# Optimization experiments

Hardware: AMD Instinct MI355X
Metric: run time of the kernel (lower is better)

The kernel has to match this reference:

```python
import jax, jax.numpy as jnp
import numpy as np

N = 50000      # nodes
E = 800000     # edges (avg degree 16)
F_IN = 128     # in_channels
H = 4          # heads
C = 32         # hidden_channels (per-head out)
L = 3          # num_layers
HC = H * C     # 128 == F_IN so residuals are active


def _layer_norm(x, g, b):
    mu = jnp.mean(x, axis=-1, keepdims=True)
    var = jnp.mean(jnp.square(x - mu), axis=-1, keepdims=True)
    return (x - mu) * jax.lax.rsqrt(var + 1e-5) * g + b


def _gatv2(x, W_l, b_l, W_r, b_r, att, src, dst, concat):
    # GATv2Conv (PyG semantics, eval mode: no dropout)
    xl = (x @ W_l + b_l).reshape(-1, H, C)   # source-side transform  [N,H,C]
    xr = (x @ W_r + b_r).reshape(-1, H, C)   # target-side transform  [N,H,C]
    e = jax.nn.leaky_relu(xl[src] + xr[dst], 0.2)          # [E,H,C]
    alpha = jnp.einsum('ehc,hc->eh', e, att)               # [E,H]
    # segment softmax over incoming edges of each dst node
    m = jax.ops.segment_max(alpha, dst, num_segments=N)    # [N,H]
    a = jnp.exp(alpha - m[dst])
    den = jax.ops.segment_sum(a, dst, num_segments=N) + 1e-16
    a = a / den[dst]
    out = jax.ops.segment_sum(xl[src] * a[:, :, None], dst, num_segments=N)  # [N,H,C]
    if concat:
        return out.reshape(N, HC)
    return out.mean(axis=1)


def setup_inputs() -> dict:
    key = jax.random.key(0)
    ks = jax.random.split(key, 6)
    s = 0.05
    return {
        "x": jax.random.normal(ks[0], (N, F_IN), jnp.float32),
        "edge_index": jax.random.randint(ks[1], (2, E), 0, N, dtype=jnp.int32),
        # all 3 layers have in=128, out=H*C=128 for the linears
        "Wl": jax.random.normal(ks[2], (L, F_IN, HC), jnp.float32) * s,
        "bl": jnp.zeros((L, HC), jnp.float32),
        "Wr": jax.random.normal(ks[3], (L, F_IN, HC), jnp.float32) * s,
        "br": jnp.zeros((L, HC), jnp.float32),
        "att": jax.random.normal(ks[4], (L, H, C), jnp.float32) * s,
        "out_bias01": jnp.zeros((2, HC), jnp.float32),   # concat layers 0,1
        "out_bias2": jnp.zeros((C,), jnp.float32),       # mean layer 2
        "ln_g01": jnp.ones((2, HC), jnp.float32),
        "ln_b01": jnp.zeros((2, HC), jnp.float32),
        "ln_g2": jnp.ones((C,), jnp.float32),
        "ln_b2": jnp.zeros((C,), jnp.float32),
    }


def reference(x, edge_index, Wl, bl, Wr, br, att,
              out_bias01, out_bias2, ln_g01, ln_b01, ln_g2, ln_b2):
    src, dst = edge_index[0], edge_index[1]
    for i in range(L):
        x_in = x
        concat = i < L - 1
        h = _gatv2(x, Wl[i], bl[i], Wr[i], br[i], att[i], src, dst, concat)
        if concat:
            h = h + out_bias01[i]
            h = _layer_norm(h, ln_g01[i], ln_b01[i])
        else:
            h = h + out_bias2
            h = _layer_norm(h, ln_g2, ln_b2)
        h = jax.nn.relu(h)  # dropout omitted (eval mode)
        if i > 0 and h.shape == x_in.shape:
            h = h + x_in
        x = h
    return x
```

## Files before the change

kernel.cpp:

```cpp
#include <hip/hip_runtime.h>
#include <math.h>


#define DPP_QP_XOR1 0xB1
#define DPP_QP_XOR2 0x4E
#define DPP_ROW_MIRROR 0x140
#define DPP_ROW_HALF_MIRROR 0x141

template <int CTRL>
__device__ __forceinline__ float dpp_add(float v) {
    int x = __builtin_amdgcn_update_dpp(0, __float_as_int(v), CTRL, 0xf, 0xf, true);
    return v + __int_as_float(x);
}

__device__ __forceinline__ unsigned bf16s(float f) {
    unsigned u = __float_as_uint(f);
    return (u + 0x7fffu + ((u >> 16) & 1u)) >> 16;
}

typedef __bf16 bf16x8 __attribute__((ext_vector_type(8)));
typedef float f32x4 __attribute__((ext_vector_type(4)));
typedef float f32x2 __attribute__((ext_vector_type(2)));


__global__ void hist_kernel(const int* __restrict__ dst, int* __restrict__ deg, int E) {
    int e = blockIdx.x * blockDim.x + threadIdx.x;
    if (e < E) atomicAdd(&deg[dst[e]], 1);
}

__global__ __launch_bounds__(256) void block_reduce_kernel(
    const int* __restrict__ deg, int* __restrict__ bsum, int Nn) {
    const int t = threadIdx.x;
    const int idx = blockIdx.x * 256 + t;
    int v = (idx < Nn) ? deg[idx] : 0;
#pragma unroll
    for (int k = 1; k <= 32; k <<= 1) v += __shfl_xor(v, k);
    __shared__ int ws[4];
    if ((t & 63) == 0) ws[t >> 6] = v;
    __syncthreads();
    if (t == 0) bsum[blockIdx.x] = ws[0] + ws[1] + ws[2] + ws[3];
}

__global__ __launch_bounds__(256) void scan_partials_kernel(
    const int* __restrict__ bsum, int* __restrict__ boff, int nb) {
    const int t = threadIdx.x;
    int v = (t < nb) ? bsum[t] : 0;
    __shared__ int s[256];
    s[t] = v;
    __syncthreads();
    for (int off = 1; off < 256; off <<= 1) {
        int u = (t >= off) ? s[t - off] : 0;
        __syncthreads();
        s[t] += u;
        __syncthreads();
    }
    if (t < nb) boff[t] = s[t] - v;
}

__global__ __launch_bounds__(256) void block_scan_write_kernel(
    const int* __restrict__ deg, const int* __restrict__ boff,
    int* __restrict__ row_start, int Nn) {
    const int t = threadIdx.x;
    const int idx = blockIdx.x * 256 + t;
    int v = (idx < Nn) ? deg[idx] : 0;
    __shared__ int s[256];
    s[t] = v;
    __syncthreads();
    for (int off = 1; off < 256; off <<= 1) {
        int u = (t >= off) ? s[t - off] : 0;
        __syncthreads();
        s[t] += u;
        __syncthreads();
    }
    if (idx < Nn) row_start[idx] = s[t] - v + boff[blockIdx.x];
}

__global__ void init_bucket_cursor(const int* __restrict__ row_start,
                                   int* __restrict__ bucket_cursor, int NB) {
    int b = blockIdx.x * blockDim.x + threadIdx.x;
    if (b < NB) bucket_cursor[b] = row_start[b * 128];
}

#define EPB 8192
#define MAXB 512

__global__ __launch_bounds__(256) void bin_kernel(
    const int* __restrict__ src, const int* __restrict__ dst,
    int* __restrict__ bucket_cursor, unsigned* __restrict__ ebuf,
    int E, int NB)
{
    __shared__ int hist[MAXB], lbase[MAXB], gbase[MAXB], cur[MAXB];
    __shared__ int sscan[256];
    __shared__ unsigned stage[EPB];
    const int t = threadIdx.x;
    const int base = blockIdx.x * EPB;
    const int cnt = min(EPB, E - base);

    for (int b = t; b < MAXB; b += 256) hist[b] = 0;
    __syncthreads();
    for (int idx = t; idx < cnt; idx += 256)
        atomicAdd(&hist[dst[base + idx] >> 7], 1);
    __syncthreads();
    {
        const int a = hist[2 * t], b = hist[2 * t + 1];
        sscan[t] = a + b;
        __syncthreads();
        for (int off = 1; off < 256; off <<= 1) {
            int u = (t >= off) ? sscan[t - off] : 0;
            __syncthreads();
            sscan[t] += u;
            __syncthreads();
        }
        const int ex = sscan[t] - (a + b);
        lbase[2 * t] = ex;
        lbase[2 * t + 1] = ex + a;
    }
    __syncthreads();
    for (int b = t; b < NB; b += 256) {
        const int c = hist[b];
        gbase[b] = (c > 0) ? atomicAdd(&bucket_cursor[b], c) : 0;
        cur[b] = lbase[b];
    }
    __syncthreads();
    for (int idx = t; idx < cnt; idx += 256) {
        const int d = dst[base + idx];
        const int bk = d >> 7;
        const int lp = atomicAdd(&cur[bk], 1);
        stage[lp] = (unsigned)src[base + idx] | ((unsigned)(d & 127) << 16)
                  | ((unsigned)bk << 23);
    }
    __syncthreads();
    for (int idx = t; idx < cnt; idx += 256) {
        const unsigned v = stage[idx];
        const int bk = v >> 23;
        ebuf[gbase[bk] + (idx - lbase[bk])] = v;
    }
}

#define BCAP 3072

__global__ __launch_bounds__(256) void place_kernel(
    const unsigned* __restrict__ ebuf, const int* __restrict__ row_start,
    int* __restrict__ src_sorted, int E, int Nn, int NB)
{
    __shared__ int cur[128];
    __shared__ unsigned short stage[BCAP];
    const int b = blockIdx.x;
    const int t = threadIdx.x;
    const int node0 = b * 128;
    const int start = row_start[node0];
    const int end = (b == NB - 1) ? E : row_start[node0 + 128];
    const int cnt = end - start;

    if (t < 128) {
        const int n = node0 + t;
        cur[t] = (n < Nn) ? row_start[n] - start : 0;
    }
    __syncthreads();

    if (cnt <= BCAP) {
        for (int i = t; i < cnt; i += 256) {
            const unsigned v = ebuf[start + i];
            const int lp = atomicAdd(&cur[(v >> 16) & 127], 1);
            stage[lp] = (unsigned short)(v & 0xffffu);
        }
        __syncthreads();
        for (int i = t; i < cnt; i += 256)
            src_sorted[start + i] = (int)stage[i];
    } else {
        for (int i = t; i < cnt; i += 256) {
            const unsigned v = ebuf[start + i];
            const int lp = atomicAdd(&cur[(v >> 16) & 127], 1);
            src_sorted[start + lp] = (int)(v & 0xffffu);
        }
    }
}


__global__ void build_bt_kernel(const float* __restrict__ Wl, const float* __restrict__ Wr,
                                unsigned short* __restrict__ Bt, int total) {
    int idx = blockIdx.x * blockDim.x + threadIdx.x;
    if (idx >= total) return;
    const int k = idx & 127;
    const int n = (idx >> 7) & 255;
    const int l = idx >> 15;
    const float v = (n < 128) ? Wl[l * 16384 + k * 128 + n]
                              : Wr[l * 16384 + k * 128 + (n - 128)];
    Bt[idx] = (unsigned short)bf16s(v);
}

__global__ void cvt_kernel(const float* __restrict__ x, unsigned* __restrict__ xb, int n8) {
    int idx = blockIdx.x * blockDim.x + threadIdx.x;
    if (idx >= n8) return;
    const float4 a = reinterpret_cast<const float4*>(x)[idx * 2];
    const float4 b = reinterpret_cast<const float4*>(x)[idx * 2 + 1];
    uint4 o;
    o.x = bf16s(a.x) | (bf16s(a.y) << 16);
    o.y = bf16s(a.z) | (bf16s(a.w) << 16);
    o.z = bf16s(b.x) | (bf16s(b.y) << 16);
    o.w = bf16s(b.z) | (bf16s(b.w) << 16);
    reinterpret_cast<uint4*>(xb)[idx] = o;
}


__global__ __launch_bounds__(256) void gemm_mfma(
    const unsigned short* __restrict__ Xb, const unsigned short* __restrict__ Bt,
    const float* __restrict__ bl, const float* __restrict__ br,
    unsigned short* __restrict__ XLb, unsigned short* __restrict__ XRb, int Nn)
{
    const int t = threadIdx.x;
    const int lane = t & 63;
    const int w = t >> 6;
    const int n0 = w * 64;
    const int l15 = lane & 15;
    const int kg = lane >> 4;
    const int rowBase = blockIdx.x * 32;

    f32x4 acc[2][4] = {};

    int ra[2];
    ra[0] = min(rowBase + l15, Nn - 1);
    ra[1] = min(rowBase + 16 + l15, Nn - 1);

#pragma unroll
    for (int ks = 0; ks < 4; ++ks) {
        const int k0 = ks * 32 + kg * 8;
        bf16x8 a[2];
        a[0] = *reinterpret_cast<const bf16x8*>(Xb + (size_t)ra[0] * 128 + k0);
        a[1] = *reinterpret_cast<const bf16x8*>(Xb + (size_t)ra[1] * 128 + k0);
#pragma unroll
        for (int nt = 0; nt < 4; ++nt) {
            const int col = n0 + nt * 16 + l15;
            const bf16x8 b = *reinterpret_cast<const bf16x8*>(Bt + (size_t)col * 128 + k0);
            acc[0][nt] = __builtin_amdgcn_mfma_f32_16x16x32_bf16(a[0], b, acc[0][nt], 0, 0, 0);
            acc[1][nt] = __builtin_amdgcn_mfma_f32_16x16x32_bf16(a[1], b, acc[1][nt], 0, 0, 0);
        }
    }

    const bool isXL = (w < 2);
#pragma unroll
    for (int mt = 0; mt < 2; ++mt) {
#pragma unroll
        for (int nt = 0; nt < 4; ++nt) {
            const int col = n0 + nt * 16 + l15;
            const float bv = isXL ? bl[col] : br[col - 128];
#pragma unroll
            for (int r = 0; r < 4; ++r) {
                const int row = rowBase + mt * 16 + kg * 4 + r;
                if (row >= Nn) continue;
                const float v = acc[mt][nt][r] + bv;
                if (isXL) XLb[(size_t)row * 128 + col] = (unsigned short)bf16s(v);
                else      XRb[(size_t)row * 128 + (col - 128)] = (unsigned short)bf16s(v);
            }
        }
    }
}


__device__ __forceinline__ void unpack8(const uint4 q, f32x2* v) {
    v[0] = f32x2{__uint_as_float(q.x << 16), __uint_as_float(q.x & 0xffff0000u)};
    v[1] = f32x2{__uint_as_float(q.y << 16), __uint_as_float(q.y & 0xffff0000u)};
    v[2] = f32x2{__uint_as_float(q.z << 16), __uint_as_float(q.z & 0xffff0000u)};
    v[3] = f32x2{__uint_as_float(q.w << 16), __uint_as_float(q.w & 0xffff0000u)};
}

__device__ __forceinline__ void edge_accum(const uint4 q, const f32x2* xr, const f32x2* av,
                                           const bool dead, float& wsum, f32x2* acc) {
    f32x2 xl[4];
    unpack8(q, xl);
    f32x2 pd = {0.f, 0.f};
#pragma unroll
    for (int j = 0; j < 4; ++j) {
        f32x2 tt = xl[j] + xr[j];
        const f32x2 u = tt * 0.2f;
        tt.x = fmaxf(tt.x, u.x);
        tt.y = fmaxf(tt.y, u.y);
        pd += tt * av[j];
    }
    float part = pd.x + pd.y;
    part = dpp_add<DPP_QP_XOR1>(part);
    part = dpp_add<DPP_QP_XOR2>(part);
    if (dead) part = -INFINITY;
    const float e = __expf(part);
    wsum += e;
    const f32x2 e2 = {e, e};
#pragma unroll
    for (int j = 0; j < 4; ++j) acc[j] += e2 * xl[j];
}

template <int MODE>
__global__ __launch_bounds__(256) void aggregate_kernel(
    const unsigned* __restrict__ XLb, const unsigned* __restrict__ XRb,
    const int* __restrict__ row_start, const int* __restrict__ deg,
    const int* __restrict__ src_sorted,
    const float* __restrict__ att, const float* __restrict__ obias,
    const float* __restrict__ lng, const float* __restrict__ lnb,
    const float* __restrict__ resid, float* __restrict__ out,
    unsigned* __restrict__ outb, int Nn)
{
    const int lane = threadIdx.x & 63;
    const int wid = threadIdx.x >> 6;
    const int node = blockIdx.x * 4 + wid;
    if (node >= Nn) return;
    const int g = lane >> 4;
    const int i = lane & 15;
    const int c0 = i * 8;

    f32x2 xr[4], av[4];
    {
        const uint4 qr = reinterpret_cast<const uint4*>(XRb)[(size_t)node * 16 + i];
        unpack8(qr, xr);
        const float4 c = *reinterpret_cast<const float4*>(att + c0);
        const float4 d = *reinterpret_cast<const float4*>(att + c0 + 4);
        av[0] = f32x2{c.x, c.y}; av[1] = f32x2{c.z, c.w};
        av[2] = f32x2{d.x, d.y}; av[3] = f32x2{d.z, d.w};
    }

    f32x2 acc[4] = {};
    float wsum = 0.f;

    const int p0 = row_start[node];
    const int dg = deg[node];
    const int p1 = p0 + dg;

    if (dg > 0) {
        int sA = src_sorted[min(p0 + g, p1 - 1)];
        int sB = src_sorted[min(p0 + 4 + g, p1 - 1)];
        for (int p = p0; p < p1; p += 8) {
            const int sAn = src_sorted[min(p + 8 + g, p1 - 1)];
            const int sBn = src_sorted[min(p + 12 + g, p1 - 1)];
            const uint4 qA = reinterpret_cast<const uint4*>(XLb)[(size_t)sA * 16 + i];
            const uint4 qB = reinterpret_cast<const uint4*>(XLb)[(size_t)sB * 16 + i];
            edge_accum(qA, xr, av, p + g >= p1, wsum, acc);
            if (p + 4 < p1)
                edge_accum(qB, xr, av, p + 4 + g >= p1, wsum, acc);
            sA = sAn;
            sB = sBn;
        }
    }

    wsum += __shfl_xor(wsum, 16); wsum += __shfl_xor(wsum, 32);
    float o[8];
#pragma unroll
    for (int j = 0; j < 4; ++j) { o[2 * j] = acc[j].x; o[2 * j + 1] = acc[j].y; }
#pragma unroll
    for (int j = 0; j < 8; ++j) {
        o[j] += __shfl_xor(o[j], 16);
        o[j] += __shfl_xor(o[j], 32);
    }

    const float inv = 1.f / (wsum + 1e-16f);
#pragma unroll
    for (int j = 0; j < 8; ++j) o[j] *= inv;

    if (MODE < 2) {
        float v[8], d[8];
        float s = 0.f;
#pragma unroll
        for (int j = 0; j < 8; ++j) { v[j] = o[j] + obias[c0 + j]; s += v[j]; }
        s = dpp_add<DPP_QP_XOR1>(s); s = dpp_add<DPP_QP_XOR2>(s);
        s = dpp_add<DPP_ROW_MIRROR>(s); s = dpp_add<DPP_ROW_HALF_MIRROR>(s);
        const float mu = s * (1.f / 128.f);
        float q = 0.f;
#pragma unroll
        for (int j = 0; j < 8; ++j) { d[j] = v[j] - mu; q = fmaf(d[j], d[j], q); }
        q = dpp_add<DPP_QP_XOR1>(q); q = dpp_add<DPP_QP_XOR2>(q);
        q = dpp_add<DPP_ROW_MIRROR>(q); q = dpp_add<DPP_ROW_HALF_MIRROR>(q);
        const float rstd = rsqrtf(q * (1.f / 128.f) + 1e-5f);
        float h[8];
#pragma unroll
        for (int j = 0; j < 8; ++j)
            h[j] = fmaxf(d[j] * rstd * lng[c0 + j] + lnb[c0 + j], 0.f);
        if (MODE == 1) {
            const float4 r0 = *reinterpret_cast<const float4*>(resid + (size_t)node * 128 + c0);
            const float4 r1 = *reinterpret_cast<const float4*>(resid + (size_t)node * 128 + c0 + 4);
            h[0] += r0.x; h[1] += r0.y; h[2] += r0.z; h[3] += r0.w;
            h[4] += r1.x; h[5] += r1.y; h[6] += r1.z; h[7] += r1.w;
        }
        if (g == 0) {
            if (MODE == 0) {
                *reinterpret_cast<float4*>(out + (size_t)node * 128 + c0) =
                    make_float4(h[0], h[1], h[2], h[3]);
                *reinterpret_cast<float4*>(out + (size_t)node * 128 + c0 + 4) =
                    make_float4(h[4], h[5], h[6], h[7]);
            }
            uint4 pb;
            pb.x = bf16s(h[0]) | (bf16s(h[1]) << 16);
            pb.y = bf16s(h[2]) | (bf16s(h[3]) << 16);
            pb.z = bf16s(h[4]) | (bf16s(h[5]) << 16);
            pb.w = bf16s(h[6]) | (bf16s(h[7]) << 16);
            reinterpret_cast<uint4*>(outb)[(size_t)node * 16 + i] = pb;
        }
    } else {
#pragma unroll
        for (int j = 0; j < 8; ++j) {
            o[j] += __shfl_xor(o[j], 4);
            o[j] += __shfl_xor(o[j], 8);
            o[j] *= 0.25f;
        }
        const int cb = (i & 3) * 8;
        float v[8], d[8];
        float s = 0.f;
#pragma unroll
        for (int j = 0; j < 8; ++j) { v[j] = o[j] + obias[cb + j]; s += v[j]; }
        s = dpp_add<DPP_QP_XOR1>(s); s = dpp_add<DPP_QP_XOR2>(s);
        const float mu = s * (1.f / 32.f);
        float q = 0.f;
#pragma unroll
        for (int j = 0; j < 8; ++j) { d[j] = v[j] - mu; q = fmaf(d[j], d[j], q); }
        q = dpp_add<DPP_QP_XOR1>(q); q = dpp_add<DPP_QP_XOR2>(q);
        const float rstd = rsqrtf(q * (1.f / 32.f) + 1e-5f);
        float h[8];
#pragma unroll
        for (int j = 0; j < 8; ++j)
            h[j] = fmaxf(d[j] * rstd * lng[cb + j] + lnb[cb + j], 0.f);
        if (lane < 4) {
            *reinterpret_cast<float4*>(out + (size_t)node * 32 + cb) =
                make_float4(h[0], h[1], h[2], h[3]);
            *reinterpret_cast<float4*>(out + (size_t)node * 32 + cb + 4) =
                make_float4(h[4], h[5], h[6], h[7]);
        }
    }
}

extern "C" void kernel_launch(void* const* d_in, const int* in_sizes, int n_in,
                              void* d_out, int out_size, void* d_ws, size_t ws_size,
                              hipStream_t stream)
{
    const float* x    = (const float*)d_in[0];
    const int*   ei   = (const int*)d_in[1];
    const float* Wl   = (const float*)d_in[2];
    const float* bl   = (const float*)d_in[3];
    const float* Wr   = (const float*)d_in[4];
    const float* br   = (const float*)d_in[5];
    const float* att  = (const float*)d_in[6];
    const float* ob01 = (const float*)d_in[7];
    const float* ob2  = (const float*)d_in[8];
    const float* lg01 = (const float*)d_in[9];
    const float* lb01 = (const float*)d_in[10];
    const float* lg2  = (const float*)d_in[11];
    const float* lb2  = (const float*)d_in[12];
    float* outp = (float*)d_out;

    const int Nn = in_sizes[0] / 128;
    const int E  = in_sizes[1] / 2;
    const int* srcI = ei;
    const int* dstI = ei + E;
    const int NB = (Nn + 127) / 128;

    char* ws = (char*)d_ws;
    size_t off = 0;
    auto alloc = [&](size_t bytes) {
        void* p = ws + off;
        off += (bytes + 255) & ~(size_t)255;
        return p;
    };
    unsigned short* Xb0  = (unsigned short*)alloc((size_t)Nn * 128 * 2);
    unsigned short* XLb  = (unsigned short*)alloc((size_t)Nn * 128 * 2);
    unsigned short* XRb  = (unsigned short*)alloc((size_t)Nn * 128 * 2);
    float* bufA          = (float*)alloc((size_t)Nn * 128 * 4);
    unsigned short* bufAb = (unsigned short*)alloc((size_t)Nn * 128 * 2);
    unsigned short* bufBb = (unsigned short*)alloc((size_t)Nn * 128 * 2);
    unsigned short* Bt   = (unsigned short*)alloc((size_t)3 * 256 * 128 * 2);
    int*   deg           = (int*)alloc((size_t)Nn * 4);
    int*   row_start     = (int*)alloc((size_t)Nn * 4);
    int*   src_sorted    = (int*)alloc((size_t)E * 4);
    unsigned* ebuf       = (unsigned*)alloc((size_t)E * 4);
    int*   bucket_cur    = (int*)alloc((size_t)MAXB * 4);
    int*   bsum          = (int*)alloc(1024 * 4);
    int*   boff          = (int*)alloc(1024 * 4);
    (void)ws_size;

    const int nb = (Nn + 255) / 256;

    hipMemsetAsync(deg, 0, (size_t)Nn * 4, stream);
    cvt_kernel<<<(Nn * 16 + 255) / 256, 256, 0, stream>>>(x, (unsigned*)Xb0, Nn * 16);
    hist_kernel<<<(E + 255) / 256, 256, 0, stream>>>(dstI, deg, E);
    build_bt_kernel<<<(3 * 256 * 128 + 255) / 256, 256, 0, stream>>>(Wl, Wr, Bt, 3 * 256 * 128);
    block_reduce_kernel<<<nb, 256, 0, stream>>>(deg, bsum, Nn);
    scan_partials_kernel<<<1, 256, 0, stream>>>(bsum, boff, nb);
    block_scan_write_kernel<<<nb, 256, 0, stream>>>(deg, boff, row_start, Nn);
    init_bucket_cursor<<<(NB + 255) / 256, 256, 0, stream>>>(row_start, bucket_cur, NB);
    bin_kernel<<<(E + EPB - 1) / EPB, 256, 0, stream>>>(srcI, dstI, bucket_cur, ebuf, E, NB);
    place_kernel<<<NB, 256, 0, stream>>>(ebuf, row_start, src_sorted, E, Nn, NB);

    const int gemm_grid = (Nn + 31) / 32;
    const int agg_grid  = (Nn + 3) / 4;

    gemm_mfma<<<gemm_grid, 256, 0, stream>>>(Xb0, Bt, bl, br, XLb, XRb, Nn);
    aggregate_kernel<0><<<agg_grid, 256, 0, stream>>>((const unsigned*)XLb, (const unsigned*)XRb,
        row_start, deg, src_sorted, att, ob01, lg01, lb01, nullptr, bufA, (unsigned*)bufAb, Nn);

    gemm_mfma<<<gemm_grid, 256, 0, stream>>>(bufAb, Bt + 32768, bl + 128, br + 128, XLb, XRb, Nn);
    aggregate_kernel<1><<<agg_grid, 256, 0, stream>>>((const unsigned*)XLb, (const unsigned*)XRb,
        row_start, deg, src_sorted, att + 128, ob01 + 128, lg01 + 128, lb01 + 128,
        bufA, nullptr, (unsigned*)bufBb, Nn);

    gemm_mfma<<<gemm_grid, 256, 0, stream>>>(bufBb, Bt + 65536, bl + 256, br + 256, XLb, XRb, Nn);
    aggregate_kernel<2><<<agg_grid, 256, 0, stream>>>((const unsigned*)XLb, (const unsigned*)XRb,
        row_start, deg, src_sorted, att + 256, ob2, lg2, lb2, nullptr, outp, nullptr, Nn);
}
```

Before: 305.4 us.

## Merge setup kernels, shrink src indices to 16-bit, read bf16 residual

Folds the bucket-cursor initialisation into the scan-write kernel and merges the x and weight bf16 conversion kernels into one prep kernel, cutting launches. Sorted source indices are stored as 16-bit values, halving index traffic in the aggregation loops, which only holds while node ids fit below 65536. The layer-1 residual now comes from the existing bf16 copy of layer-0 output rather than a separate fp32 buffer, so the fp32 write and read go away at the cost of extra rounding in the residual. The leaky-relu uses a vector max builtin.

```diff
diff --git a/kernel.cpp b/kernel.cpp
--- a/kernel.cpp
+++ b/kernel.cpp
@@ -59,7 +59,7 @@
 
 __global__ __launch_bounds__(256) void block_scan_write_kernel(
     const int* __restrict__ deg, const int* __restrict__ boff,
-    int* __restrict__ row_start, int Nn) {
+    int* __restrict__ row_start, int* __restrict__ bucket_cursor, int Nn) {
     const int t = threadIdx.x;
     const int idx = blockIdx.x * 256 + t;
     int v = (idx < Nn) ? deg[idx] : 0;
@@ -72,13 +72,11 @@
         s[t] += u;
         __syncthreads();
     }
-    if (idx < Nn) row_start[idx] = s[t] - v + boff[blockIdx.x];
-}
-
-__global__ void init_bucket_cursor(const int* __restrict__ row_start,
-                                   int* __restrict__ bucket_cursor, int NB) {
-    int b = blockIdx.x * blockDim.x + threadIdx.x;
-    if (b < NB) bucket_cursor[b] = row_start[b * 128];
+    if (idx < Nn) {
+        const int ex = s[t] - v + boff[blockIdx.x];
+        row_start[idx] = ex;
+        if ((idx & 127) == 0) bucket_cursor[idx >> 7] = ex;
+    }
 }
 
 #define EPB 8192
@@ -141,7 +139,7 @@
 
 __global__ __launch_bounds__(256) void place_kernel(
     const unsigned* __restrict__ ebuf, const int* __restrict__ row_start,
-    int* __restrict__ src_sorted, int E, int Nn, int NB)
+    unsigned short* __restrict__ src_sorted, int E, int Nn, int NB)
 {
     __shared__ int cur[128];
     __shared__ unsigned short stage[BCAP];
@@ -166,40 +164,41 @@
         }
         __syncthreads();
         for (int i = t; i < cnt; i += 256)
-            src_sorted[start + i] = (int)stage[i];
+            src_sorted[start + i] = stage[i];
     } else {
         for (int i = t; i < cnt; i += 256) {
             const unsigned v = ebuf[start + i];
             const int lp = atomicAdd(&cur[(v >> 16) & 127], 1);
-            src_sorted[start + lp] = (int)(v & 0xffffu);
-        }
-    }
-}
-
-
-__global__ void build_bt_kernel(const float* __restrict__ Wl, const float* __restrict__ Wr,
-                                unsigned short* __restrict__ Bt, int total) {
-    int idx = blockIdx.x * blockDim.x + threadIdx.x;
-    if (idx >= total) return;
-    const int k = idx & 127;
-    const int n = (idx >> 7) & 255;
-    const int l = idx >> 15;
-    const float v = (n < 128) ? Wl[l * 16384 + k * 128 + n]
-                              : Wr[l * 16384 + k * 128 + (n - 128)];
-    Bt[idx] = (unsigned short)bf16s(v);
-}
-
-__global__ void cvt_kernel(const float* __restrict__ x, unsigned* __restrict__ xb, int n8) {
-    int idx = blockIdx.x * blockDim.x + threadIdx.x;
-    if (idx >= n8) return;
-    const float4 a = reinterpret_cast<const float4*>(x)[idx * 2];
-    const float4 b = reinterpret_cast<const float4*>(x)[idx * 2 + 1];
-    uint4 o;
-    o.x = bf16s(a.x) | (bf16s(a.y) << 16);
-    o.y = bf16s(a.z) | (bf16s(a.w) << 16);
-    o.z = bf16s(b.x) | (bf16s(b.y) << 16);
-    o.w = bf16s(b.z) | (bf16s(b.w) << 16);
-    reinterpret_cast<uint4*>(xb)[idx] = o;
+            src_sorted[start + lp] = (unsigned short)(v & 0xffffu);
+        }
+    }
+}
+
+
+__global__ __launch_bounds__(256) void prep_kernel(
+    const float* __restrict__ x, const float* __restrict__ Wl,
+    const float* __restrict__ Wr, unsigned* __restrict__ xb,
+    unsigned short* __restrict__ Bt, int n8, int btTotal)
+{
+    const int idx = blockIdx.x * blockDim.x + threadIdx.x;
+    if (idx < n8) {
+        const float4 a = reinterpret_cast<const float4*>(x)[idx * 2];
+        const float4 b = reinterpret_cast<const float4*>(x)[idx * 2 + 1];
+        uint4 o;
+        o.x = bf16s(a.x) | (bf16s(a.y) << 16);
+        o.y = bf16s(a.z) | (bf16s(a.w) << 16);
+        o.z = bf16s(b.x) | (bf16s(b.y) << 16);
+        o.w = bf16s(b.z) | (bf16s(b.w) << 16);
+        reinterpret_cast<uint4*>(xb)[idx] = o;
+    }
+    if (idx < btTotal) {
+        const int k = idx & 127;
+        const int n = (idx >> 7) & 255;
+        const int l = idx >> 15;
+        const float v = (n < 128) ? Wl[l * 16384 + k * 128 + n]
+                                  : Wr[l * 16384 + k * 128 + (n - 128)];
+        Bt[idx] = (unsigned short)bf16s(v);
+    }
 }
 
 
@@ -272,9 +271,7 @@
 #pragma unroll
     for (int j = 0; j < 4; ++j) {
         f32x2 tt = xl[j] + xr[j];
-        const f32x2 u = tt * 0.2f;
-        tt.x = fmaxf(tt.x, u.x);
-        tt.y = fmaxf(tt.y, u.y);
+        tt = __builtin_elementwise_max(tt, tt * 0.2f);
         pd += tt * av[j];
     }
     float part = pd.x + pd.y;
@@ -292,10 +289,10 @@
 __global__ __launch_bounds__(256) void aggregate_kernel(
     const unsigned* __restrict__ XLb, const unsigned* __restrict__ XRb,
     const int* __restrict__ row_start, const int* __restrict__ deg,
-    const int* __restrict__ src_sorted,
+    const unsigned short* __restrict__ src_sorted,
     const float* __restrict__ att, const float* __restrict__ obias,
     const float* __restrict__ lng, const float* __restrict__ lnb,
-    const float* __restrict__ resid, float* __restrict__ out,
+    const unsigned* __restrict__ residb, float* __restrict__ out,
     unsigned* __restrict__ outb, int Nn)
 {
     const int lane = threadIdx.x & 63;
@@ -372,18 +369,13 @@
         for (int j = 0; j < 8; ++j)
             h[j] = fmaxf(d[j] * rstd * lng[c0 + j] + lnb[c0 + j], 0.f);
         if (MODE == 1) {
-            const float4 r0 = *reinterpret_cast<const float4*>(resid + (size_t)node * 128 + c0);
-            const float4 r1 = *reinterpret_cast<const float4*>(resid + (size_t)node * 128 + c0 + 4);
-            h[0] += r0.x; h[1] += r0.y; h[2] += r0.z; h[3] += r0.w;
-            h[4] += r1.x; h[5] += r1.y; h[6] += r1.z; h[7] += r1.w;
+            const uint4 qr2 = reinterpret_cast<const uint4*>(residb)[(size_t)node * 16 + i];
+            f32x2 rr[4];
+            unpack8(qr2, rr);
+            h[0] += rr[0].x; h[1] += rr[0].y; h[2] += rr[1].x; h[3] += rr[1].y;
+            h[4] += rr[2].x; h[5] += rr[2].y; h[6] += rr[3].x; h[7] += rr[3].y;
         }
         if (g == 0) {
-            if (MODE == 0) {
-                *reinterpret_cast<float4*>(out + (size_t)node * 128 + c0) =
-                    make_float4(h[0], h[1], h[2], h[3]);
-                *reinterpret_cast<float4*>(out + (size_t)node * 128 + c0 + 4) =
-                    make_float4(h[4], h[5], h[6], h[7]);
-            }
             uint4 pb;
             pb.x = bf16s(h[0]) | (bf16s(h[1]) << 16);
             pb.y = bf16s(h[2]) | (bf16s(h[3]) << 16);
@@ -455,32 +447,31 @@
         off += (bytes + 255) & ~(size_t)255;
         return p;
     };
-    unsigned short* Xb0  = (unsigned short*)alloc((size_t)Nn * 128 * 2);
-    unsigned short* XLb  = (unsigned short*)alloc((size_t)Nn * 128 * 2);
-    unsigned short* XRb  = (unsigned short*)alloc((size_t)Nn * 128 * 2);
-    float* bufA          = (float*)alloc((size_t)Nn * 128 * 4);
+    unsigned short* Xb0   = (unsigned short*)alloc((size_t)Nn * 128 * 2);
+    unsigned short* XLb   = (unsigned short*)alloc((size_t)Nn * 128 * 2);
+    unsigned short* XRb   = (unsigned short*)alloc((size_t)Nn * 128 * 2);
     unsigned short* bufAb = (unsigned short*)alloc((size_t)Nn * 128 * 2);
     unsigned short* bufBb = (unsigned short*)alloc((size_t)Nn * 128 * 2);
-    unsigned short* Bt   = (unsigned short*)alloc((size_t)3 * 256 * 128 * 2);
-    int*   deg           = (int*)alloc((size_t)Nn * 4);
-    int*   row_start     = (int*)alloc((size_t)Nn * 4);
-    int*   src_sorted    = (int*)alloc((size_t)E * 4);
-    unsigned* ebuf       = (unsigned*)alloc((size_t)E * 4);
-    int*   bucket_cur    = (int*)alloc((size_t)MAXB * 4);
-    int*   bsum          = (int*)alloc(1024 * 4);
-    int*   boff          = (int*)alloc(1024 * 4);
+    unsigned short* Bt    = (unsigned short*)alloc((size_t)3 * 256 * 128 * 2);
+    int*   deg            = (int*)alloc((size_t)Nn * 4);
+    int*   row_start      = (int*)alloc((size_t)Nn * 4);
+    unsigned short* src_sorted = (unsigned short*)alloc((size_t)E * 2 + 64);
+    unsigned* ebuf        = (unsigned*)alloc((size_t)E * 4);
+    int*   bucket_cur     = (int*)alloc((size_t)MAXB * 4);
+    int*   bsum           = (int*)alloc(1024 * 4);
+    int*   boff           = (int*)alloc(1024 * 4);
     (void)ws_size;
 
     const int nb = (Nn + 255) / 256;
+    const int btTotal = 3 * 256 * 128;
 
     hipMemsetAsync(deg, 0, (size_t)Nn * 4, stream);
-    cvt_kernel<<<(Nn * 16 + 255) / 256, 256, 0, stream>>>(x, (unsigned*)Xb0, Nn * 16);
+    prep_kernel<<<(Nn * 16 + 255) / 256, 256, 0, stream>>>(x, Wl, Wr, (unsigned*)Xb0, Bt,
+                                                           Nn * 16, btTotal);
     hist_kernel<<<(E + 255) / 256, 256, 0, stream>>>(dstI, deg, E);
-    build_bt_kernel<<<(3 * 256 * 128 + 255) / 256, 256, 0, stream>>>(Wl, Wr, Bt, 3 * 256 * 128);
     block_reduce_kernel<<<nb, 256, 0, stream>>>(deg, bsum, Nn);
     scan_partials_kernel<<<1, 256, 0, stream>>>(bsum, boff, nb);
-    block_scan_write_kernel<<<nb, 256, 0, stream>>>(deg, boff, row_start, Nn);
-    init_bucket_cursor<<<(NB + 255) / 256, 256, 0, stream>>>(row_start, bucket_cur, NB);
+    block_scan_write_kernel<<<nb, 256, 0, stream>>>(deg, boff, row_start, bucket_cur, Nn);
     bin_kernel<<<(E + EPB - 1) / EPB, 256, 0, stream>>>(srcI, dstI, bucket_cur, ebuf, E, NB);
     place_kernel<<<NB, 256, 0, stream>>>(ebuf, row_start, src_sorted, E, Nn, NB);
 
@@ -489,12 +480,13 @@
 
     gemm_mfma<<<gemm_grid, 256, 0, stream>>>(Xb0, Bt, bl, br, XLb, XRb, Nn);
     aggregate_kernel<0><<<agg_grid, 256, 0, stream>>>((const unsigned*)XLb, (const unsigned*)XRb,
-        row_start, deg, src_sorted, att, ob01, lg01, lb01, nullptr, bufA, (unsigned*)bufAb, Nn);
+        row_start, deg, src_sorted, att, ob01, lg01, lb01, nullptr, nullptr,
+        (unsigned*)bufAb, Nn);
 
     gemm_mfma<<<gemm_grid, 256, 0, stream>>>(bufAb, Bt + 32768, bl + 128, br + 128, XLb, XRb, Nn);
     aggregate_kernel<1><<<agg_grid, 256, 0, stream>>>((const unsigned*)XLb, (const unsigned*)XRb,
         row_start, deg, src_sorted, att + 128, ob01 + 128, lg01 + 128, lb01 + 128,
-        bufA, nullptr, (unsigned*)bufBb, Nn);
+        (const unsigned*)bufAb, nullptr, (unsigned*)bufBb, Nn);
 
     gemm_mfma<<<gemm_grid, 256, 0, stream>>>(bufBb, Bt + 65536, bl + 256, br + 256, XLb, XRb, Nn);
     aggregate_kernel<2><<<agg_grid, 256, 0, stream>>>((const unsigned*)XLb, (const unsigned*)XRb,
```

New measurement: 300.8 us. No clear change (-1.5%).
